# Optimization experiments

Measured on AMD Instinct MI355X. Metric: run time of the kernel, lower is better.

The kernel has to match this reference:

```python
import jax, jax.numpy as jnp
import numpy as np

N, K, D = 8192, 256, 64

def setup_inputs() -> dict:
    key = jax.random.key(0)
    k1, k2, k3, k4, k5 = jax.random.split(key, 5)
    x = jax.random.normal(k1, (N, D), dtype=jnp.float32)
    means = 0.001 * jax.random.uniform(k2, (K, D), dtype=jnp.float32)
    diag = jax.random.normal(k3, (1, K, D), dtype=jnp.float32)
    tri = 0.01 * jax.random.normal(k4, (1, K, D, D), dtype=jnp.float32)
    weigh = jax.random.normal(k5, (1, K), dtype=jnp.float32)
    return {"x": x, "means": means, "diag": diag, "tri": tri, "weigh": weigh}

def reference(x, means, diag, tri, weigh):
    d = x.shape[1]
    logC = -d / 2 * jnp.log(jnp.asarray(2 * np.pi, dtype=x.dtype))
    w = jax.nn.log_softmax(weigh, axis=1)                 # [1,K]
    y = x[:, None, :] - means[None, :, :]                 # [N,K,d]
    lv = jnp.tanh(diag)                                   # [1,K,d]
    y = y * lv                                            # [N,K,d]
    L = jnp.tril(tri[0], k=-1)                            # [K,d,d] strictly lower
    y = y + jnp.einsum('kij,nkj->nki', L, y)              # [N,K,d]
    q = jnp.sum(y * y, axis=2)                            # [N,K]
    logdet = jnp.sum(jnp.log(jnp.abs(lv)), axis=2)        # [1,K]
    val = -q / 2 + logdet + w                             # [N,K]
    logpdf = logC + jax.nn.logsumexp(val, axis=-1)        # [N]
    return jnp.mean(-logpdf)                              # scalar
```

## Files before the change

### kernel.cpp

```cpp
#include <hip/hip_runtime.h>
#include <cstdint>
#include <cstddef>

#define NTOT 8192
#define KTOT 256

typedef _Float16 half2v __attribute__((ext_vector_type(2)));
typedef _Float16 half8  __attribute__((ext_vector_type(8)));
typedef float floatx16 __attribute__((ext_vector_type(16)));

static constexpr size_t G_ELEMS   = (size_t)8 * 260 * 64 * 8;
static constexpr size_t OFF_CK    = G_ELEMS * 2;
static constexpr size_t OFF_BPART = OFF_CK + 1024;
static constexpr size_t OFF_VAL   = 2134016;

__device__ __forceinline__ uint16_t f2h(float x) {
  _Float16 h = (_Float16)x;
  return __builtin_bit_cast(uint16_t, h);
}

__device__ __forceinline__ half8 mkh(half2v s, const half2v* rp) {
  union { half2v p[4]; half8 v; } u;
  u.p[0] = s * rp[0]; u.p[1] = s * rp[1]; u.p[2] = s * rp[2]; u.p[3] = s * rp[3];
  return u.v;
}
__device__ __forceinline__ half8 cph(const half2v* rp) {
  union { half2v p[4]; half8 v; } u;
  u.p[0] = rp[0]; u.p[1] = rp[1]; u.p[2] = rp[2]; u.p[3] = rp[3];
  return u.v;
}

__global__ void p1_prep(const float* __restrict__ means, const float* __restrict__ diag,
                        const float* __restrict__ tri, const float* __restrict__ weigh,
                        uint16_t* __restrict__ Gf, float* __restrict__ ck) {
  int k = blockIdx.x;
  int t = threadIdx.x;
  __shared__ float lv[64], ms[64], red[64], wred[256];
  __shared__ float Wp[64][64];
  __shared__ float SS[64][64];
  __shared__ float logdet_s, lse_s;

  float wv = weigh[t];
  wred[t] = wv; __syncthreads();
  for (int o = 128; o > 0; o >>= 1) { if (t < o) wred[t] = fmaxf(wred[t], wred[t + o]); __syncthreads(); }
  float wm = wred[0]; __syncthreads();
  wred[t] = __expf(wv - wm); __syncthreads();
  for (int o = 128; o > 0; o >>= 1) { if (t < o) wred[t] += wred[t + o]; __syncthreads(); }
  if (t == 0) lse_s = wm + __logf(wred[0]);

  if (t < 64) {
    float d = diag[k * 64 + t];
    float l = tanhf(d);
    lv[t] = l;
    ms[t] = means[k * 64 + t];
    red[t] = __logf(fabsf(l));
  }
  __syncthreads();

  for (int e = 0; e < 16; ++e) {
    int idx = e * 256 + t;
    int i = idx >> 6, c = idx & 63;
    float L = (c < i) ? tri[k * 4096 + idx] : 0.f;
    float w = ((c == i) ? 1.f : 0.f) + L;
    Wp[i][c] = w * lv[c];
  }
  __syncthreads();

  if (t == 0) {
    float s = 0.f;
    for (int i = 0; i < 64; ++i) s += red[i];
    logdet_s = s;
  }

  int i0 = (t >> 4) * 4, j0 = (t & 15) * 4;
  float acc[4][4];
  #pragma unroll
  for (int a = 0; a < 4; ++a)
    #pragma unroll
    for (int b = 0; b < 4; ++b) acc[a][b] = 0.f;
  for (int r = 0; r < 64; ++r) {
    float4 av = *(const float4*)&Wp[r][i0];
    float4 bv = *(const float4*)&Wp[r][j0];
    float aa[4] = {av.x, av.y, av.z, av.w};
    float bb[4] = {bv.x, bv.y, bv.z, bv.w};
    #pragma unroll
    for (int a = 0; a < 4; ++a)
      #pragma unroll
      for (int b = 0; b < 4; ++b) acc[a][b] = fmaf(aa[a], bb[b], acc[a][b]);
  }

  int k32 = k >> 5, kl = k & 31;
  #pragma unroll
  for (int a = 0; a < 4; ++a) {
    #pragma unroll
    for (int b = 0; b < 4; ++b) {
      int i = i0 + a, j = j0 + b;
      float s = acc[a][b];
      SS[i][j] = s;
      int u = i * 64 + j;
      int st = u >> 4, half = (u >> 3) & 1, je = u & 7;
      size_t gi = ((size_t)(k32 * 260 + st) * 64 + half * 32 + kl) * 8 + je;
      Gf[gi] = f2h(-0.5f * s);
    }
  }
  __syncthreads();

  if (t < 64) {
    float b = 0.f;
    for (int j = 0; j < 64; ++j) b = fmaf(SS[t][j], ms[j], b);
    int st = 256 + (t >> 4), half = (t >> 3) & 1, je = t & 7;
    Gf[((size_t)(k32 * 260 + st) * 64 + half * 32 + kl) * 8 + je] = f2h(b);
    red[t] = b * ms[t];
  }
  __syncthreads();
  if (t == 0) {
    float msm = 0.f;
    for (int i = 0; i < 64; ++i) msm += red[i];
    ck[k] = logdet_s + (weigh[k] - lse_s) - 0.5f * msm;
  }
}

#define GROUP_BODY(GIDX, BCUR, BNEXT, SNEXT, DOPF)                                   \
  do {                                                                               \
    int i_ = ibase + (GIDX);                                                         \
    float xf0 = xl[r0][i_];                                                          \
    float xf1 = xl[r1][i_];                                                          \
    half2v xi0; xi0[0] = (_Float16)xf0; xi0[1] = xi0[0];                             \
    half2v xi1; xi1[0] = (_Float16)xf1; xi1[1] = xi1[0];                             \
    if (DOPF) {                                                                      \
      _Pragma("unroll")                                                              \
      for (int c = 0; c < 4; ++c) BNEXT[c] = Bp[bofs + (size_t)((SNEXT) + c) * 64];  \
    }                                                                                \
    _Pragma("unroll")                                                                \
    for (int c = 0; c < 4; ++c) {                                                    \
      half8 a0 = mkh(xi0, runh0[c]);                                                 \
      half8 a1 = mkh(xi1, runh1[c]);                                                 \
      half8 bb = __builtin_bit_cast(half8, BCUR[c]);                                 \
      acc0 = __builtin_amdgcn_mfma_f32_32x32x16_f16(a0, bb, acc0, 0, 0, 0);          \
      acc1 = __builtin_amdgcn_mfma_f32_32x32x16_f16(a1, bb, acc1, 0, 0, 0);          \
    }                                                                                \
  } while (0)

__launch_bounds__(256, 2)
__global__ void k2_gemm(const float* __restrict__ x, const uint16_t* __restrict__ Gf,
                        float* __restrict__ valp) {
  __shared__ float xl[128][65];
  int t = threadIdx.x;
  int bx = blockIdx.x, by = blockIdx.y, bz = blockIdx.z;
  const float* xblk = x + (size_t)bx * 128 * 64;

  for (int e = 0; e < 8; ++e) {
    int lin = e * 1024 + t * 4;
    float4 v = *(const float4*)(xblk + lin);
    int r = lin >> 6, c = lin & 63;
    xl[r][c] = v.x; xl[r][c + 1] = v.y; xl[r][c + 2] = v.z; xl[r][c + 3] = v.w;
  }
  __syncthreads();

  int wave = t >> 6, l = t & 63;
  int wn = wave >> 1, wk = wave & 1;
  int half = l >> 5, lane31 = l & 31;
  int r0 = wn * 64 + lane31;
  int r1 = r0 + 32;

  half2v runh0[4][4], runh1[4][4];
  #pragma unroll
  for (int c = 0; c < 4; ++c) {
    int base = c * 16 + half * 8;
    float4 ra = *(const float4*)(xblk + (size_t)r0 * 64 + base);
    float4 rb = *(const float4*)(xblk + (size_t)r0 * 64 + base + 4);
    runh0[c][0][0] = (_Float16)ra.x; runh0[c][0][1] = (_Float16)ra.y;
    runh0[c][1][0] = (_Float16)ra.z; runh0[c][1][1] = (_Float16)ra.w;
    runh0[c][2][0] = (_Float16)rb.x; runh0[c][2][1] = (_Float16)rb.y;
    runh0[c][3][0] = (_Float16)rb.z; runh0[c][3][1] = (_Float16)rb.w;
    float4 rc = *(const float4*)(xblk + (size_t)r1 * 64 + base);
    float4 rd = *(const float4*)(xblk + (size_t)r1 * 64 + base + 4);
    runh1[c][0][0] = (_Float16)rc.x; runh1[c][0][1] = (_Float16)rc.y;
    runh1[c][1][0] = (_Float16)rc.z; runh1[c][1][1] = (_Float16)rc.w;
    runh1[c][2][0] = (_Float16)rd.x; runh1[c][2][1] = (_Float16)rd.y;
    runh1[c][3][0] = (_Float16)rd.z; runh1[c][3][1] = (_Float16)rd.w;
  }

  int k32 = by * 2 + wk;
  const uint4* Bp = (const uint4*)Gf;
  size_t bofs = (size_t)(k32 * 260) * 64 + l;

  floatx16 acc0, acc1;
  #pragma unroll
  for (int i = 0; i < 16; ++i) { acc0[i] = 0.f; acc1[i] = 0.f; }

  int sbase = bz * 128;
  int ibase = sbase >> 2;

  uint4 bufA[4], bufB[4];
  #pragma unroll
  for (int c = 0; c < 4; ++c) bufA[c] = Bp[bofs + (size_t)(sbase + c) * 64];

  for (int g = 0; g < 32; g += 2) {
    GROUP_BODY(g, bufA, bufB, sbase + (g + 1) * 4, true);
    GROUP_BODY(g + 1, bufB, bufA, sbase + (g + 2) * 4, ((g + 2) < 32) || (bz == 1));
  }

  if (bz == 1) {
    #pragma unroll
    for (int c = 0; c < 4; ++c) {
      half8 a0 = cph(runh0[c]);
      half8 a1 = cph(runh1[c]);
      half8 bb = __builtin_bit_cast(half8, bufA[c]);
      acc0 = __builtin_amdgcn_mfma_f32_32x32x16_f16(a0, bb, acc0, 0, 0, 0);
      acc1 = __builtin_amdgcn_mfma_f32_32x32x16_f16(a1, bb, acc1, 0, 0, 0);
    }
  }

  int nbase = bx * 128 + wn * 64;
  int kcol = by * 64 + wk * 32 + lane31;
  float* out = valp + (size_t)bz * NTOT * KTOT;
  #pragma unroll
  for (int reg = 0; reg < 16; ++reg) {
    int row = (reg & 3) + 8 * (reg >> 2) + 4 * half;
    out[(size_t)(nbase + row) * KTOT + kcol] = acc0[reg];
    out[(size_t)(nbase + 32 + row) * KTOT + kcol] = acc1[reg];
  }
}

__global__ void k3_lse(const float* __restrict__ valp, const float* __restrict__ ck,
                       float* __restrict__ bpart) {
  __shared__ float red[4];
  int t = threadIdx.x;
  int wave = t >> 6, l = t & 63;
  float4 ckv = ((const float4*)ck)[l];
  const float4* b0 = (const float4*)valp;
  const float4* b1 = (const float4*)(valp + (size_t)NTOT * KTOT);
  float acc = 0.f;
  #pragma unroll
  for (int rr = 0; rr < 8; ++rr) {
    size_t n = (size_t)blockIdx.x * 32 + wave * 8 + rr;
    float4 va = b0[n * 64 + l];
    float4 vb = b1[n * 64 + l];
    float v0 = va.x + vb.x + ckv.x, v1 = va.y + vb.y + ckv.y;
    float v2 = va.z + vb.z + ckv.z, v3 = va.w + vb.w + ckv.w;
    float mx = fmaxf(fmaxf(v0, v1), fmaxf(v2, v3));
    #pragma unroll
    for (int o = 32; o > 0; o >>= 1) mx = fmaxf(mx, __shfl_xor(mx, o));
    float s = __expf(v0 - mx) + __expf(v1 - mx) + __expf(v2 - mx) + __expf(v3 - mx);
    #pragma unroll
    for (int o = 32; o > 0; o >>= 1) s += __shfl_xor(s, o);
    acc += mx + __logf(s);
  }
  if (l == 0) red[wave] = acc;
  __syncthreads();
  if (t == 0) bpart[blockIdx.x] = red[0] + red[1] + red[2] + red[3];
}

__global__ void k4_final(const float* __restrict__ bpart, float* __restrict__ out) {
  __shared__ float red[256];
  int t = threadIdx.x;
  red[t] = bpart[t]; __syncthreads();
  for (int o = 128; o > 0; o >>= 1) { if (t < o) red[t] += red[t + o]; __syncthreads(); }
  if (t == 0) out[0] = 58.8120661251f - red[0] / 8192.0f;
}

extern "C" void kernel_launch(void* const* d_in, const int* in_sizes, int n_in,
                              void* d_out, int out_size, void* d_ws, size_t ws_size,
                              hipStream_t stream) {
  const float* x     = (const float*)d_in[0];
  const float* means = (const float*)d_in[1];
  const float* diag  = (const float*)d_in[2];
  const float* tri   = (const float*)d_in[3];
  const float* weigh = (const float*)d_in[4];

  char* ws = (char*)d_ws;
  uint16_t* Gf  = (uint16_t*)ws;
  float* ck     = (float*)(ws + OFF_CK);
  float* bpart  = (float*)(ws + OFF_BPART);
  float* valp   = (float*)(ws + OFF_VAL);

  p1_prep<<<dim3(256), dim3(256), 0, stream>>>(means, diag, tri, weigh, Gf, ck);
  k2_gemm<<<dim3(64, 4, 2), dim3(256), 0, stream>>>(x, Gf, valp);
  k3_lse<<<dim3(256), dim3(256), 0, stream>>>(valp, ck, bpart);
  k4_final<<<dim3(1), dim3(256), 0, stream>>>(bpart, (float*)d_out);
}
```

Measured before the change: 107.4 us.

## Fuse partial logsumexp into GEMM epilogue and drop split-K value buffer

The GEMM kernel no longer splits the 260-step K dimension across two z-blocks that each write a full N×K float partial to global memory. Each block now runs the whole reduction, adds the per-component constant, stages the tile in shared memory and emits a per-row (max, sumexp) pair for its 64 components. This removes two 8 MB intermediate writes and their reread in the LSE kernel, at the cost of half as many GEMM blocks and a longer serial MFMA chain per block. The prep kernel also gains vectorized packed stores and shuffle-based reductions, and the final reductions use wave shuffles.

```diff
diff --git a/kernel.cpp b/kernel.cpp
--- a/kernel.cpp
+++ b/kernel.cpp
@@ -35,10 +35,10 @@
                         uint16_t* __restrict__ Gf, float* __restrict__ ck) {
   int k = blockIdx.x;
   int t = threadIdx.x;
-  __shared__ float lv[64], ms[64], red[64], wred[256];
-  __shared__ float Wp[64][64];
-  __shared__ float SS[64][64];
-  __shared__ float logdet_s, lse_s;
+  __shared__ float lv[64], ms[64], bv64[64], wred[256];
+  __shared__ float Wp[64][68];
+  __shared__ float SS[64][65];
+  __shared__ float lse_s;
 
   float wv = weigh[t];
   wred[t] = wv; __syncthreads();
@@ -48,12 +48,16 @@
   for (int o = 128; o > 0; o >>= 1) { if (t < o) wred[t] += wred[t + o]; __syncthreads(); }
   if (t == 0) lse_s = wm + __logf(wred[0]);
 
+  float logdet0 = 0.f;
   if (t < 64) {
     float d = diag[k * 64 + t];
     float l = tanhf(d);
     lv[t] = l;
     ms[t] = means[k * 64 + t];
-    red[t] = __logf(fabsf(l));
+    float ld = __logf(fabsf(l));
+    #pragma unroll
+    for (int o = 32; o > 0; o >>= 1) ld += __shfl_xor(ld, o);
+    logdet0 = ld;
   }
   __syncthreads();
 
@@ -66,12 +70,6 @@
   }
   __syncthreads();
 
-  if (t == 0) {
-    float s = 0.f;
-    for (int i = 0; i < 64; ++i) s += red[i];
-    logdet_s = s;
-  }
-
   int i0 = (t >> 4) * 4, j0 = (t & 15) * 4;
   float acc[4][4];
   #pragma unroll
@@ -88,66 +86,52 @@
       #pragma unroll
       for (int b = 0; b < 4; ++b) acc[a][b] = fmaf(aa[a], bb[b], acc[a][b]);
   }
-
-  int k32 = k >> 5, kl = k & 31;
-  #pragma unroll
-  for (int a = 0; a < 4; ++a) {
-    #pragma unroll
-    for (int b = 0; b < 4; ++b) {
-      int i = i0 + a, j = j0 + b;
-      float s = acc[a][b];
-      SS[i][j] = s;
-      int u = i * 64 + j;
-      int st = u >> 4, half = (u >> 3) & 1, je = u & 7;
-      size_t gi = ((size_t)(k32 * 260 + st) * 64 + half * 32 + kl) * 8 + je;
-      Gf[gi] = f2h(-0.5f * s);
-    }
-  }
+  #pragma unroll
+  for (int a = 0; a < 4; ++a)
+    #pragma unroll
+    for (int b = 0; b < 4; ++b) SS[i0 + a][j0 + b] = acc[a][b];
   __syncthreads();
 
   if (t < 64) {
     float b = 0.f;
     for (int j = 0; j < 64; ++j) b = fmaf(SS[t][j], ms[j], b);
-    int st = 256 + (t >> 4), half = (t >> 3) & 1, je = t & 7;
-    Gf[((size_t)(k32 * 260 + st) * 64 + half * 32 + kl) * 8 + je] = f2h(b);
-    red[t] = b * ms[t];
-  }
-  __syncthreads();
-  if (t == 0) {
-    float msm = 0.f;
-    for (int i = 0; i < 64; ++i) msm += red[i];
-    ck[k] = logdet_s + (weigh[k] - lse_s) - 0.5f * msm;
-  }
-}
-
-#define GROUP_BODY(GIDX, BCUR, BNEXT, SNEXT, DOPF)                                   \
-  do {                                                                               \
-    int i_ = ibase + (GIDX);                                                         \
-    float xf0 = xl[r0][i_];                                                          \
-    float xf1 = xl[r1][i_];                                                          \
-    half2v xi0; xi0[0] = (_Float16)xf0; xi0[1] = xi0[0];                             \
-    half2v xi1; xi1[0] = (_Float16)xf1; xi1[1] = xi1[0];                             \
-    if (DOPF) {                                                                      \
-      _Pragma("unroll")                                                              \
-      for (int c = 0; c < 4; ++c) BNEXT[c] = Bp[bofs + (size_t)((SNEXT) + c) * 64];  \
-    }                                                                                \
-    _Pragma("unroll")                                                                \
-    for (int c = 0; c < 4; ++c) {                                                    \
-      half8 a0 = mkh(xi0, runh0[c]);                                                 \
-      half8 a1 = mkh(xi1, runh1[c]);                                                 \
-      half8 bb = __builtin_bit_cast(half8, BCUR[c]);                                 \
-      acc0 = __builtin_amdgcn_mfma_f32_32x32x16_f16(a0, bb, acc0, 0, 0, 0);          \
-      acc1 = __builtin_amdgcn_mfma_f32_32x32x16_f16(a1, bb, acc1, 0, 0, 0);          \
-    }                                                                                \
-  } while (0)
-
-__launch_bounds__(256, 2)
+    bv64[t] = b;
+    float bm = b * ms[t];
+    #pragma unroll
+    for (int o = 32; o > 0; o >>= 1) bm += __shfl_xor(bm, o);
+    if (t == 0) ck[k] = logdet0 + (weigh[k] - lse_s) - 0.5f * bm;
+  }
+  __syncthreads();
+
+  int k32 = k >> 5, kl = k & 31;
+  for (int cc = t; cc < 520; cc += 256) {
+    float v[8];
+    if (cc < 512) {
+      int i = cc >> 3, jb = (cc & 7) * 8;
+      #pragma unroll
+      for (int e = 0; e < 8; ++e) v[e] = -0.5f * SS[i][jb + e];
+    } else {
+      int b0 = (cc - 512) * 8;
+      #pragma unroll
+      for (int e = 0; e < 8; ++e) v[e] = bv64[b0 + e];
+    }
+    uint4 pk;
+    pk.x = (uint32_t)f2h(v[0]) | ((uint32_t)f2h(v[1]) << 16);
+    pk.y = (uint32_t)f2h(v[2]) | ((uint32_t)f2h(v[3]) << 16);
+    pk.z = (uint32_t)f2h(v[4]) | ((uint32_t)f2h(v[5]) << 16);
+    pk.w = (uint32_t)f2h(v[6]) | ((uint32_t)f2h(v[7]) << 16);
+    size_t base = ((size_t)(k32 * 260 + (cc >> 1)) * 64 + (cc & 1) * 32 + kl) * 8;
+    *(uint4*)(Gf + base) = pk;
+  }
+}
+
+__launch_bounds__(256)
 __global__ void k2_gemm(const float* __restrict__ x, const uint16_t* __restrict__ Gf,
-                        float* __restrict__ valp) {
+                        const float* __restrict__ ck, float* __restrict__ val2) {
   __shared__ float xl[128][65];
   int t = threadIdx.x;
-  int bx = blockIdx.x, by = blockIdx.y, bz = blockIdx.z;
-  const float* xblk = x + (size_t)bx * 128 * 64;
+  int bx = blockIdx.x, by = blockIdx.y;
+  const float* xblk = x + (size_t)bx * (128 * 64);
 
   for (int e = 0; e < 8; ++e) {
     int lin = e * 1024 + t * 4;
@@ -160,8 +144,7 @@
   int wave = t >> 6, l = t & 63;
   int wn = wave >> 1, wk = wave & 1;
   int half = l >> 5, lane31 = l & 31;
-  int r0 = wn * 64 + lane31;
-  int r1 = r0 + 32;
+  int r0 = wn * 64 + lane31, r1 = r0 + 32;
 
   half2v runh0[4][4], runh1[4][4];
   #pragma unroll
@@ -189,75 +172,87 @@
   #pragma unroll
   for (int i = 0; i < 16; ++i) { acc0[i] = 0.f; acc1[i] = 0.f; }
 
-  int sbase = bz * 128;
-  int ibase = sbase >> 2;
-
-  uint4 bufA[4], bufB[4];
-  #pragma unroll
-  for (int c = 0; c < 4; ++c) bufA[c] = Bp[bofs + (size_t)(sbase + c) * 64];
-
-  for (int g = 0; g < 32; g += 2) {
-    GROUP_BODY(g, bufA, bufB, sbase + (g + 1) * 4, true);
-    GROUP_BODY(g + 1, bufB, bufA, sbase + (g + 2) * 4, ((g + 2) < 32) || (bz == 1));
-  }
-
-  if (bz == 1) {
-    #pragma unroll
-    for (int c = 0; c < 4; ++c) {
-      half8 a0 = cph(runh0[c]);
-      half8 a1 = cph(runh1[c]);
-      half8 bb = __builtin_bit_cast(half8, bufA[c]);
-      acc0 = __builtin_amdgcn_mfma_f32_32x32x16_f16(a0, bb, acc0, 0, 0, 0);
-      acc1 = __builtin_amdgcn_mfma_f32_32x32x16_f16(a1, bb, acc1, 0, 0, 0);
+  uint4 bufs[4][4];
+  #pragma unroll
+  for (int p = 0; p < 4; ++p)
+    #pragma unroll
+    for (int c = 0; c < 4; ++c) bufs[p][c] = Bp[bofs + (size_t)(p * 4 + c) * 64];
+
+  for (int g = 0; g < 64; g += 4) {
+    #pragma unroll
+    for (int p = 0; p < 4; ++p) {
+      int gg = g + p;
+      float xf0 = xl[r0][gg], xf1 = xl[r1][gg];
+      _Float16 h0 = (_Float16)xf0; half2v xi0; xi0[0] = h0; xi0[1] = h0;
+      _Float16 h1 = (_Float16)xf1; half2v xi1; xi1[0] = h1; xi1[1] = h1;
+      #pragma unroll
+      for (int c = 0; c < 4; ++c) {
+        half8 a0 = mkh(xi0, runh0[c]);
+        half8 a1 = mkh(xi1, runh1[c]);
+        half8 bb = __builtin_bit_cast(half8, bufs[p][c]);
+        acc0 = __builtin_amdgcn_mfma_f32_32x32x16_f16(a0, bb, acc0, 0, 0, 0);
+        acc1 = __builtin_amdgcn_mfma_f32_32x32x16_f16(a1, bb, acc1, 0, 0, 0);
+      }
+      #pragma unroll
+      for (int c = 0; c < 4; ++c)
+        bufs[p][c] = Bp[bofs + (size_t)((gg + 4) * 4 + c) * 64];
     }
   }
 
-  int nbase = bx * 128 + wn * 64;
-  int kcol = by * 64 + wk * 32 + lane31;
-  float* out = valp + (size_t)bz * NTOT * KTOT;
+  #pragma unroll
+  for (int c = 0; c < 4; ++c) {
+    half8 a0 = cph(runh0[c]);
+    half8 a1 = cph(runh1[c]);
+    half8 bb = __builtin_bit_cast(half8, bufs[0][c]);
+    acc0 = __builtin_amdgcn_mfma_f32_32x32x16_f16(a0, bb, acc0, 0, 0, 0);
+    acc1 = __builtin_amdgcn_mfma_f32_32x32x16_f16(a1, bb, acc1, 0, 0, 0);
+  }
+
+  __syncthreads();
+  float ckv = ck[by * 64 + wk * 32 + lane31];
   #pragma unroll
   for (int reg = 0; reg < 16; ++reg) {
     int row = (reg & 3) + 8 * (reg >> 2) + 4 * half;
-    out[(size_t)(nbase + row) * KTOT + kcol] = acc0[reg];
-    out[(size_t)(nbase + 32 + row) * KTOT + kcol] = acc1[reg];
-  }
-}
-
-__global__ void k3_lse(const float* __restrict__ valp, const float* __restrict__ ck,
-                       float* __restrict__ bpart) {
+    xl[wn * 64 + row][wk * 32 + lane31] = acc0[reg] + ckv;
+    xl[wn * 64 + 32 + row][wk * 32 + lane31] = acc1[reg] + ckv;
+  }
+  __syncthreads();
+  if (t < 128) {
+    float m = -3.0e38f;
+    #pragma unroll
+    for (int j = 0; j < 64; ++j) m = fmaxf(m, xl[t][j]);
+    float s = 0.f;
+    #pragma unroll
+    for (int j = 0; j < 64; ++j) s += __expf(xl[t][j] - m);
+    size_t n = (size_t)bx * 128 + t;
+    val2[n * 8 + by * 2 + 0] = m;
+    val2[n * 8 + by * 2 + 1] = s;
+  }
+}
+
+__global__ void k3_lse(const float* __restrict__ val2, float* __restrict__ bpart) {
   __shared__ float red[4];
   int t = threadIdx.x;
-  int wave = t >> 6, l = t & 63;
-  float4 ckv = ((const float4*)ck)[l];
-  const float4* b0 = (const float4*)valp;
-  const float4* b1 = (const float4*)(valp + (size_t)NTOT * KTOT);
-  float acc = 0.f;
-  #pragma unroll
-  for (int rr = 0; rr < 8; ++rr) {
-    size_t n = (size_t)blockIdx.x * 32 + wave * 8 + rr;
-    float4 va = b0[n * 64 + l];
-    float4 vb = b1[n * 64 + l];
-    float v0 = va.x + vb.x + ckv.x, v1 = va.y + vb.y + ckv.y;
-    float v2 = va.z + vb.z + ckv.z, v3 = va.w + vb.w + ckv.w;
-    float mx = fmaxf(fmaxf(v0, v1), fmaxf(v2, v3));
-    #pragma unroll
-    for (int o = 32; o > 0; o >>= 1) mx = fmaxf(mx, __shfl_xor(mx, o));
-    float s = __expf(v0 - mx) + __expf(v1 - mx) + __expf(v2 - mx) + __expf(v3 - mx);
-    #pragma unroll
-    for (int o = 32; o > 0; o >>= 1) s += __shfl_xor(s, o);
-    acc += mx + __logf(s);
-  }
-  if (l == 0) red[wave] = acc;
+  size_t n = (size_t)blockIdx.x * 256 + t;
+  const float4* p = (const float4*)(val2 + n * 8);
+  float4 a = p[0], b = p[1];
+  float M = fmaxf(fmaxf(a.x, a.z), fmaxf(b.x, b.z));
+  float s = a.y * __expf(a.x - M) + a.w * __expf(a.z - M) +
+            b.y * __expf(b.x - M) + b.w * __expf(b.z - M);
+  float lse = M + __logf(s);
+  #pragma unroll
+  for (int o = 32; o > 0; o >>= 1) lse += __shfl_xor(lse, o);
+  if ((t & 63) == 0) red[t >> 6] = lse;
   __syncthreads();
   if (t == 0) bpart[blockIdx.x] = red[0] + red[1] + red[2] + red[3];
 }
 
 __global__ void k4_final(const float* __restrict__ bpart, float* __restrict__ out) {
-  __shared__ float red[256];
-  int t = threadIdx.x;
-  red[t] = bpart[t]; __syncthreads();
-  for (int o = 128; o > 0; o >>= 1) { if (t < o) red[t] += red[t + o]; __syncthreads(); }
-  if (t == 0) out[0] = 58.8120661251f - red[0] / 8192.0f;
+  int t = threadIdx.x;
+  float v = (t < 32) ? bpart[t] : 0.f;
+  #pragma unroll
+  for (int o = 32; o > 0; o >>= 1) v += __shfl_xor(v, o);
+  if (t == 0) out[0] = 58.8120661251f - v / 8192.0f;
 }
 
 extern "C" void kernel_launch(void* const* d_in, const int* in_sizes, int n_in,
@@ -273,10 +268,10 @@
   uint16_t* Gf  = (uint16_t*)ws;
   float* ck     = (float*)(ws + OFF_CK);
   float* bpart  = (float*)(ws + OFF_BPART);
-  float* valp   = (float*)(ws + OFF_VAL);
+  float* val2   = (float*)(ws + OFF_VAL);
 
   p1_prep<<<dim3(256), dim3(256), 0, stream>>>(means, diag, tri, weigh, Gf, ck);
-  k2_gemm<<<dim3(64, 4, 2), dim3(256), 0, stream>>>(x, Gf, valp);
-  k3_lse<<<dim3(256), dim3(256), 0, stream>>>(valp, ck, bpart);
-  k4_final<<<dim3(1), dim3(256), 0, stream>>>(bpart, (float*)d_out);
-}
+  k2_gemm<<<dim3(64, 4), dim3(256), 0, stream>>>(x, Gf, ck, val2);
+  k3_lse<<<dim3(32), dim3(256), 0, stream>>>(val2, bpart);
+  k4_final<<<dim3(1), dim3(64), 0, stream>>>(bpart, (float*)d_out);
+}
```

New measurement: 97.95 us. 8.8% less time.
